# Kernel optimization log

Measured on AMD Instinct MI355X. Metric: run time of the kernel, lower is better.

## Reference

```python
import jax, jax.numpy as jnp
import numpy as np
from jax import lax

B, C, N = 8, 3, 65536
NUM_POINTS = 1024


def setup_inputs() -> dict:
    key = jax.random.key(0)
    points = jax.random.normal(key, (B, C, N), dtype=jnp.float32)
    return {"points": points}


def furthest_point_sampling(xyz, num_points):
    # xyz: (B, N, 3) -> indices (B, num_points), int32
    b, n, _ = xyz.shape
    init_idx = jnp.zeros((b,), dtype=jnp.int32)  # CUDA FPS seeds with index 0
    init_dists = jnp.full((b, n), 1e10, dtype=xyz.dtype)

    def step(carry, _):
        dists, last_idx = carry
        last_pt = jnp.take_along_axis(xyz, last_idx[:, None, None], axis=1)  # (B,1,3)
        d = jnp.sum(jnp.square(xyz - last_pt), axis=-1)  # (B,N) squared dist to newest pt
        dists = jnp.minimum(dists, d)
        nxt = jnp.argmax(dists, axis=-1).astype(jnp.int32)
        return (dists, nxt), nxt

    (_, _), rest = lax.scan(step, (init_dists, init_idx), None, length=num_points - 1)
    # rest: (num_points-1, B) -> (B, num_points)
    idx = jnp.concatenate([init_idx[None, :], rest], axis=0).T
    return idx


def reference(points):
    # points: (B, 3, N), channels-first as in the torch module
    xyz = jnp.transpose(points, (0, 2, 1))  # (B, N, 3)
    idx = furthest_point_sampling(xyz, NUM_POINTS)  # (B, num_points)
    # fps_gather_by_index: gather along point axis of (B, 3, N)
    new_points = jnp.take_along_axis(points, idx[:, None, :], axis=2)  # (B, 3, num_points)
    return new_points
```

## Files before the change

kernel.cpp:

```cpp
#include <hip/hip_runtime.h>


namespace {

constexpr int kB = 8;
constexpr int kN = 65536;
constexpr int kNP = 1024;
constexpr int kPB = 16;
constexpr int kThreads = 256;
constexpr int kPPT = kN / (kPB * kThreads);
constexpr int kGrp = kPPT / 4;
constexpr int kWaves = kThreads / 64;
constexpr int kRgn = 16;
constexpr int kRgnStride = 32;
constexpr int kBlocks = 256;

__device__ __forceinline__ unsigned long long shfl_xor_u64(unsigned long long v, int off) {
  return (unsigned long long)__shfl_xor((long long)v, off, 64);
}

__device__ __forceinline__ unsigned long long u64max(unsigned long long a,
                                                     unsigned long long b) {
  return a > b ? a : b;
}

__device__ __forceinline__ unsigned long long load_l2(const unsigned long long* p) {
  unsigned long long v;
  asm volatile("global_load_dwordx2 %0, %1, off sc0\n\ts_waitcnt vmcnt(0)"
               : "=v"(v)
               : "v"(p)
               : "memory");
  return v;
}

__device__ __forceinline__ void store_l2(unsigned long long* p, unsigned long long v) {
  asm volatile("global_store_dwordx2 %0, %1, off sc0" ::"v"(p), "v"(v) : "memory");
}

__global__ __launch_bounds__(kThreads) void fps_kernel(const float* __restrict__ pts,
                                                       float* __restrict__ out,
                                                       unsigned long long* __restrict__ slots,
                                                       unsigned* __restrict__ ctrl) {
  const int tid = threadIdx.x;
  const int lane = tid & 63;
  const int wave = tid >> 6;

  __shared__ int s_batch, s_slice;
  __shared__ unsigned long long s_wkey[kWaves];
  __shared__ unsigned s_win[2];
  __shared__ int s_hist[kNP];

  if (tid == 0) {
    unsigned xcc;
    asm volatile("s_getreg_b32 %0, hwreg(HW_REG_XCC_ID)" : "=s"(xcc));
    const int home = (int)(xcc & 7u);
    int batch = -1, slice = -1;
    const int pos = (int)atomicAdd(&ctrl[home], 1u);
    if (pos < kPB) {
      batch = home;
      slice = pos;
    }
    __hip_atomic_fetch_add(&ctrl[8], 1u, __ATOMIC_RELEASE, __HIP_MEMORY_SCOPE_AGENT);
    if (batch < 0) {
      while (__hip_atomic_load(&ctrl[8], __ATOMIC_ACQUIRE, __HIP_MEMORY_SCOPE_AGENT) <
             (unsigned)kBlocks) {
        __builtin_amdgcn_s_sleep(8);
      }
      int need = (int)atomicAdd(&ctrl[9], 1u);
      for (int j = 0; j < kB; ++j) {
        int have = (int)__hip_atomic_load(&ctrl[j], __ATOMIC_RELAXED, __HIP_MEMORY_SCOPE_AGENT);
        have = have > kPB ? kPB : have;
        const int vac = kPB - have;
        if (need < vac) {
          batch = j;
          slice = have + need;
          break;
        }
        need -= vac;
      }
    }
    s_batch = batch;
    s_slice = slice;
    s_win[0] = 0xFFFFFFFFu;
    s_win[1] = 0xFFFFFFFFu;
  }
  __syncthreads();

  const int batch = s_batch;
  const int slice = s_slice;
  if (batch < 0) return;

  const float* __restrict__ xb = pts + (size_t)batch * 3 * kN;
  const float* __restrict__ yb = xb + kN;
  const float* __restrict__ zb = xb + 2 * kN;

  const int sbase = slice * (kThreads * kPPT);
  const int base0 = sbase + tid * 4;
  float px[kPPT], py[kPPT], pz[kPPT], dist[kPPT];
#pragma unroll
  for (int g = 0; g < kGrp; ++g) {
    const int base = base0 + g * (kThreads * 4);
    const float4 vx = *reinterpret_cast<const float4*>(xb + base);
    const float4 vy = *reinterpret_cast<const float4*>(yb + base);
    const float4 vz = *reinterpret_cast<const float4*>(zb + base);
    px[g * 4 + 0] = vx.x; px[g * 4 + 1] = vx.y; px[g * 4 + 2] = vx.z; px[g * 4 + 3] = vx.w;
    py[g * 4 + 0] = vy.x; py[g * 4 + 1] = vy.y; py[g * 4 + 2] = vy.z; py[g * 4 + 3] = vy.w;
    pz[g * 4 + 0] = vz.x; pz[g * 4 + 1] = vz.y; pz[g * 4 + 2] = vz.z; pz[g * 4 + 3] = vz.w;
  }
#pragma unroll
  for (int k = 0; k < kPPT; ++k) dist[k] = 1e10f;

  float qx = xb[0], qy = yb[0], qz = zb[0];

  unsigned long long* const sb = slots + (size_t)batch * kRgn * kRgnStride;

  for (int it = 1; it < kNP; ++it) {
    float bd = -1.0f;
    int bi = 0;
#pragma unroll
    for (int g = 0; g < kGrp; ++g) {
#pragma unroll
      for (int j = 0; j < 4; ++j) {
        const int k = g * 4 + j;
        const float dx = px[k] - qx;
        const float dy = py[k] - qy;
        const float dz = pz[k] - qz;
        const float ss =
            __fadd_rn(__fadd_rn(__fmul_rn(dx, dx), __fmul_rn(dy, dy)), __fmul_rn(dz, dz));
        const float nd = fminf(dist[k], ss);
        dist[k] = nd;
        if (nd > bd) {
          bd = nd;
          bi = base0 + g * (kThreads * 4) + j;
        }
      }
    }

    unsigned long long key = ((unsigned long long)__float_as_uint(bd) << 32) |
                             ((unsigned long long)(0xFFFFu - (unsigned)bi) << 16) |
                             (unsigned long long)(unsigned)it;

#pragma unroll
    for (int off = 32; off > 0; off >>= 1) {
      key = u64max(key, shfl_xor_u64(key, off));
    }
    if (lane == 0) s_wkey[wave] = key;
    __syncthreads();

    int wi;
    if (wave == 0) {
      unsigned long long bk = s_wkey[lane & (kWaves - 1)];
#pragma unroll
      for (int off = 1; off < kWaves; off <<= 1) {
        bk = u64max(bk, shfl_xor_u64(bk, off));
      }

      unsigned long long* const rgn = sb + (size_t)(it & (kRgn - 1)) * kRgnStride;
      if (lane == 0) {
        store_l2(rgn + slice, bk);
        __hip_atomic_store(rgn + kPB + slice, bk, __ATOMIC_RELAXED,
                           __HIP_MEMORY_SCOPE_AGENT);
      }

      unsigned long long w;
      int round = 0;
      for (;;) {
        unsigned long long a = load_l2(rgn + (lane & (kPB - 1)));
        bool ok = (unsigned)(a & 0xFFFFull) == (unsigned)it;
        if (round >= 2 && !ok) {
          const unsigned long long fb = __hip_atomic_load(
              rgn + kPB + (lane & (kPB - 1)), __ATOMIC_RELAXED, __HIP_MEMORY_SCOPE_AGENT);
          if ((unsigned)(fb & 0xFFFFull) == (unsigned)it) {
            a = fb;
            ok = true;
          }
        }
        if (__all(ok)) {
          w = a;
          break;
        }
        ++round;
      }
#pragma unroll
      for (int off = 1; off < kPB; off <<= 1) {
        w = u64max(w, shfl_xor_u64(w, off));
      }
      wi = (int)(0xFFFFu - ((unsigned)(w >> 16) & 0xFFFFu));
      if (lane == 0) {
        s_hist[it] = wi;
        __hip_atomic_store(&s_win[it & 1], ((unsigned)wi << 16) | (unsigned)it,
                           __ATOMIC_RELAXED, __HIP_MEMORY_SCOPE_WORKGROUP);
      }
    } else {
      unsigned v;
      do {
        v = __hip_atomic_load(&s_win[it & 1], __ATOMIC_RELAXED, __HIP_MEMORY_SCOPE_WORKGROUP);
      } while ((v & 0xFFFFu) != (unsigned)it);
      wi = (int)(v >> 16);
    }

    const int wiu = __builtin_amdgcn_readfirstlane(wi);
    qx = xb[wiu];
    qy = yb[wiu];
    qz = zb[wiu];
  }

  __syncthreads();

  if (slice == 0) {
    float* __restrict__ ob = out + (size_t)batch * 3 * kNP;
    for (int j = tid; j < kNP; j += kThreads) {
      const int id = (j == 0) ? 0 : s_hist[j];
      ob[j] = xb[id];
      ob[kNP + j] = yb[id];
      ob[2 * kNP + j] = zb[id];
    }
  }
}

}

extern "C" void kernel_launch(void* const* d_in, const int* in_sizes, int n_in,
                              void* d_out, int out_size, void* d_ws, size_t ws_size,
                              hipStream_t stream) {
  (void)in_sizes;
  (void)n_in;
  (void)out_size;
  (void)ws_size;
  const float* pts = (const float*)d_in[0];
  float* out = (float*)d_out;
  unsigned* ctrl = (unsigned*)d_ws;
  unsigned long long* slots = (unsigned long long*)((char*)d_ws + 1024);
  hipMemsetAsync(d_ws, 0, 64, stream);
  fps_kernel<<<dim3(kBlocks), dim3(kThreads), 0, stream>>>(pts, out, slots, ctrl);
}
```

Before: 1.663 ms.

## Publish per-wave keys globally and drop intra-block barrier and LDS handoff

Each wave now writes its own reduced key into a global slot array (16 slices x 4 waves = 64 slots), and every wave independently polls all 64 slots and reduces them. This removes the per-iteration __syncthreads, the wave-0-only cross-block exchange and the LDS spin handoff to the other waves. Each lane also prefetches the coordinates of its candidate speculatively, and the winner's coordinates are broadcast with a shuffle, so the dependent global load is taken off the critical path. The cost is four times more L2 polling traffic per block, and the ring depth drops from 16 to 8 regions.

```diff
diff --git a/kernel.cpp b/kernel.cpp
--- a/kernel.cpp
+++ b/kernel.cpp
@@ -11,9 +11,11 @@
 constexpr int kPPT = kN / (kPB * kThreads);
 constexpr int kGrp = kPPT / 4;
 constexpr int kWaves = kThreads / 64;
-constexpr int kRgn = 16;
-constexpr int kRgnStride = 32;
-constexpr int kBlocks = 256;
+constexpr int kSlots = kPB * kWaves;
+constexpr int kRgn = 8;
+constexpr int kRgnStride = 2 * kSlots;
+constexpr int kBatchStride = kRgn * kRgnStride;
+constexpr int kBlocks = kB * kPB;
 
 __device__ __forceinline__ unsigned long long shfl_xor_u64(unsigned long long v, int off) {
   return (unsigned long long)__shfl_xor((long long)v, off, 64);
@@ -46,8 +48,6 @@
   const int wave = tid >> 6;
 
   __shared__ int s_batch, s_slice;
-  __shared__ unsigned long long s_wkey[kWaves];
-  __shared__ unsigned s_win[2];
   __shared__ int s_hist[kNP];
 
   if (tid == 0) {
@@ -81,8 +81,6 @@
     }
     s_batch = batch;
     s_slice = slice;
-    s_win[0] = 0xFFFFFFFFu;
-    s_win[1] = 0xFFFFFFFFu;
   }
   __syncthreads();
 
@@ -112,7 +110,8 @@
 
   float qx = xb[0], qy = yb[0], qz = zb[0];
 
-  unsigned long long* const sb = slots + (size_t)batch * kRgn * kRgnStride;
+  unsigned long long* const sb = slots + (size_t)batch * kBatchStride;
+  const int slot = slice * kWaves + wave;
 
   for (int it = 1; it < kNP; ++it) {
     float bd = -1.0f;
@@ -144,65 +143,52 @@
     for (int off = 32; off > 0; off >>= 1) {
       key = u64max(key, shfl_xor_u64(key, off));
     }
-    if (lane == 0) s_wkey[wave] = key;
-    __syncthreads();
-
-    int wi;
-    if (wave == 0) {
-      unsigned long long bk = s_wkey[lane & (kWaves - 1)];
-#pragma unroll
-      for (int off = 1; off < kWaves; off <<= 1) {
-        bk = u64max(bk, shfl_xor_u64(bk, off));
-      }
-
-      unsigned long long* const rgn = sb + (size_t)(it & (kRgn - 1)) * kRgnStride;
-      if (lane == 0) {
-        store_l2(rgn + slice, bk);
-        __hip_atomic_store(rgn + kPB + slice, bk, __ATOMIC_RELAXED,
-                           __HIP_MEMORY_SCOPE_AGENT);
-      }
-
-      unsigned long long w;
-      int round = 0;
-      for (;;) {
-        unsigned long long a = load_l2(rgn + (lane & (kPB - 1)));
-        bool ok = (unsigned)(a & 0xFFFFull) == (unsigned)it;
-        if (round >= 2 && !ok) {
-          const unsigned long long fb = __hip_atomic_load(
-              rgn + kPB + (lane & (kPB - 1)), __ATOMIC_RELAXED, __HIP_MEMORY_SCOPE_AGENT);
-          if ((unsigned)(fb & 0xFFFFull) == (unsigned)it) {
-            a = fb;
-            ok = true;
-          }
+
+    unsigned long long* const rgn = sb + (size_t)(it & (kRgn - 1)) * kRgnStride;
+
+    if (lane == 0) {
+      store_l2(rgn + slot, key);
+      __hip_atomic_store(rgn + kSlots + slot, key, __ATOMIC_RELAXED,
+                         __HIP_MEMORY_SCOPE_AGENT);
+    }
+
+    unsigned long long w;
+    int round = 0;
+    for (;;) {
+      unsigned long long a = load_l2(rgn + lane);
+      bool ok = (unsigned)(a & 0xFFFFull) == (unsigned)it;
+      if (round >= 2 && !ok) {
+        const unsigned long long fb = __hip_atomic_load(
+            rgn + kSlots + lane, __ATOMIC_RELAXED, __HIP_MEMORY_SCOPE_AGENT);
+        if ((unsigned)(fb & 0xFFFFull) == (unsigned)it) {
+          a = fb;
+          ok = true;
         }
-        if (__all(ok)) {
-          w = a;
-          break;
-        }
-        ++round;
-      }
-#pragma unroll
-      for (int off = 1; off < kPB; off <<= 1) {
-        w = u64max(w, shfl_xor_u64(w, off));
-      }
-      wi = (int)(0xFFFFu - ((unsigned)(w >> 16) & 0xFFFFu));
-      if (lane == 0) {
-        s_hist[it] = wi;
-        __hip_atomic_store(&s_win[it & 1], ((unsigned)wi << 16) | (unsigned)it,
-                           __ATOMIC_RELAXED, __HIP_MEMORY_SCOPE_WORKGROUP);
-      }
-    } else {
-      unsigned v;
-      do {
-        v = __hip_atomic_load(&s_win[it & 1], __ATOMIC_RELAXED, __HIP_MEMORY_SCOPE_WORKGROUP);
-      } while ((v & 0xFFFFu) != (unsigned)it);
-      wi = (int)(v >> 16);
-    }
-
-    const int wiu = __builtin_amdgcn_readfirstlane(wi);
-    qx = xb[wiu];
-    qy = yb[wiu];
-    qz = zb[wiu];
+      }
+      if (__all(ok)) {
+        w = a;
+        break;
+      }
+      ++round;
+    }
+
+    const int cand = (int)(0xFFFFu - ((unsigned)(w >> 16) & 0xFFFFu));
+    const float gx = xb[cand];
+    const float gy = yb[cand];
+    const float gz = zb[cand];
+
+    unsigned long long k2 = w;
+#pragma unroll
+    for (int off = 32; off > 0; off >>= 1) {
+      k2 = u64max(k2, shfl_xor_u64(k2, off));
+    }
+
+    const int src = (int)__ffsll((unsigned long long)__ballot(k2 == w)) - 1;
+    qx = __shfl(gx, src, 64);
+    qy = __shfl(gy, src, 64);
+    qz = __shfl(gz, src, 64);
+
+    if (tid == 0) s_hist[it] = (int)(0xFFFFu - ((unsigned)(k2 >> 16) & 0xFFFFu));
   }
 
   __syncthreads();
```

Measured after the change: 1.830 ms. +10.0%, slower.

## Use DPP reductions and prefetch candidate coordinates before final cross-block max

Applied to the files above, without the earlier changes.

Replaces the ds_swizzle/shfl-based 64-bit max reductions with DPP row operations plus readlane, which shortens the per-iteration intra-wave reduction. Wave 0 now loads the coordinates of every slice's candidate in parallel, overlapping that latency with the final reduction, and picks the winner's coordinates with ballot/readlane. It then broadcasts them to the other waves through shared memory with release/acquire ordering, so those waves no longer issue a dependent global load. This removes a serial global-memory round trip from the critical path of every iteration. It adds complexity in DPP control codes and in the cross-lane selection logic.

```diff
diff --git a/kernel.cpp b/kernel.cpp
--- a/kernel.cpp
+++ b/kernel.cpp
@@ -15,13 +15,14 @@
 constexpr int kRgnStride = 32;
 constexpr int kBlocks = 256;
 
-__device__ __forceinline__ unsigned long long shfl_xor_u64(unsigned long long v, int off) {
-  return (unsigned long long)__shfl_xor((long long)v, off, 64);
-}
-
-__device__ __forceinline__ unsigned long long u64max(unsigned long long a,
-                                                     unsigned long long b) {
-  return a > b ? a : b;
+template <int CTRL>
+__device__ __forceinline__ unsigned long long dpp_max_u64(unsigned long long k) {
+  const int lo = (int)(unsigned)k;
+  const int hi = (int)(unsigned)(k >> 32);
+  const unsigned plo = (unsigned)__builtin_amdgcn_update_dpp(lo, lo, CTRL, 0xF, 0xF, false);
+  const unsigned phi = (unsigned)__builtin_amdgcn_update_dpp(hi, hi, CTRL, 0xF, 0xF, false);
+  const unsigned long long p = ((unsigned long long)phi << 32) | plo;
+  return p > k ? p : k;
 }
 
 __device__ __forceinline__ unsigned long long load_l2(const unsigned long long* p) {
@@ -48,6 +49,7 @@
   __shared__ int s_batch, s_slice;
   __shared__ unsigned long long s_wkey[kWaves];
   __shared__ unsigned s_win[2];
+  __shared__ float s_qc[2][3];
   __shared__ int s_hist[kNP];
 
   if (tid == 0) {
@@ -140,20 +142,23 @@
                              ((unsigned long long)(0xFFFFu - (unsigned)bi) << 16) |
                              (unsigned long long)(unsigned)it;
 
-#pragma unroll
-    for (int off = 32; off > 0; off >>= 1) {
-      key = u64max(key, shfl_xor_u64(key, off));
-    }
-    if (lane == 0) s_wkey[wave] = key;
+    key = dpp_max_u64<0x111>(key);
+    key = dpp_max_u64<0x112>(key);
+    key = dpp_max_u64<0x114>(key);
+    key = dpp_max_u64<0x118>(key);
+    key = dpp_max_u64<0x142>(key);
+    key = dpp_max_u64<0x143>(key);
+    const unsigned wklo = (unsigned)__builtin_amdgcn_readlane((int)(unsigned)key, 63);
+    const unsigned wkhi = (unsigned)__builtin_amdgcn_readlane((int)(unsigned)(key >> 32), 63);
+    if (lane == 0) {
+      s_wkey[wave] = ((unsigned long long)wkhi << 32) | wklo;
+    }
     __syncthreads();
 
-    int wi;
     if (wave == 0) {
       unsigned long long bk = s_wkey[lane & (kWaves - 1)];
-#pragma unroll
-      for (int off = 1; off < kWaves; off <<= 1) {
-        bk = u64max(bk, shfl_xor_u64(bk, off));
-      }
+      bk = dpp_max_u64<0xB1>(bk);
+      bk = dpp_max_u64<0x4E>(bk);
 
       unsigned long long* const rgn = sb + (size_t)(it & (kRgn - 1)) * kRgnStride;
       if (lane == 0) {
@@ -162,7 +167,7 @@
                            __HIP_MEMORY_SCOPE_AGENT);
       }
 
-      unsigned long long w;
+      unsigned long long sv;
       int round = 0;
       for (;;) {
         unsigned long long a = load_l2(rgn + (lane & (kPB - 1)));
@@ -176,33 +181,47 @@
           }
         }
         if (__all(ok)) {
-          w = a;
+          sv = a;
           break;
         }
         ++round;
       }
-#pragma unroll
-      for (int off = 1; off < kPB; off <<= 1) {
-        w = u64max(w, shfl_xor_u64(w, off));
-      }
-      wi = (int)(0xFFFFu - ((unsigned)(w >> 16) & 0xFFFFu));
+
+      const int cand = (int)(0xFFFFu - ((unsigned)(sv >> 16) & 0xFFFFu));
+      const float gx = xb[cand];
+      const float gy = yb[cand];
+      const float gz = zb[cand];
+
+      unsigned long long k2 = sv;
+      k2 = dpp_max_u64<0xB1>(k2);
+      k2 = dpp_max_u64<0x4E>(k2);
+      k2 = dpp_max_u64<0x141>(k2);
+      k2 = dpp_max_u64<0x140>(k2);
+
+      const unsigned long long m = __ballot(sv == k2);
+      const int src = (int)__ffsll(m) - 1;
+      qx = __int_as_float(__builtin_amdgcn_readlane(__float_as_int(gx), src));
+      qy = __int_as_float(__builtin_amdgcn_readlane(__float_as_int(gy), src));
+      qz = __int_as_float(__builtin_amdgcn_readlane(__float_as_int(gz), src));
+
+      const int wi = (int)(0xFFFFu - ((unsigned)(k2 >> 16) & 0xFFFFu));
       if (lane == 0) {
         s_hist[it] = wi;
+        s_qc[it & 1][0] = qx;
+        s_qc[it & 1][1] = qy;
+        s_qc[it & 1][2] = qz;
         __hip_atomic_store(&s_win[it & 1], ((unsigned)wi << 16) | (unsigned)it,
-                           __ATOMIC_RELAXED, __HIP_MEMORY_SCOPE_WORKGROUP);
+                           __ATOMIC_RELEASE, __HIP_MEMORY_SCOPE_WORKGROUP);
       }
     } else {
       unsigned v;
       do {
-        v = __hip_atomic_load(&s_win[it & 1], __ATOMIC_RELAXED, __HIP_MEMORY_SCOPE_WORKGROUP);
+        v = __hip_atomic_load(&s_win[it & 1], __ATOMIC_ACQUIRE, __HIP_MEMORY_SCOPE_WORKGROUP);
       } while ((v & 0xFFFFu) != (unsigned)it);
-      wi = (int)(v >> 16);
-    }
-
-    const int wiu = __builtin_amdgcn_readfirstlane(wi);
-    qx = xb[wiu];
-    qy = yb[wiu];
-    qz = zb[wiu];
+      qx = s_qc[it & 1][0];
+      qy = s_qc[it & 1][1];
+      qz = s_qc[it & 1][2];
+    }
   }
 
   __syncthreads();
```

Result: faster. 1.489 ms (-10.5%).
